# Kernel optimization log

Hardware: AMD Instinct MI355X
Metric: run time of the kernel (lower is better)

Reference implementation:

```python
import jax, jax.numpy as jnp
import numpy as np

B, D, E, H, O, TOP_K = 65536, 256, 16, 256, 256, 2
GATE_T = 1.0  # gate_temperature default


def setup_inputs() -> dict:
    key = jax.random.key(0)
    ks = jax.random.split(key, 8)
    sn = lambda k, shape, sc: (jax.random.normal(k, shape, jnp.float32) * sc)
    return {
        "x": sn(ks[0], (B, D), 1.0),
        # per-expert input bias, init N(0, 0.02) as in the module
        "bias": sn(ks[1], (E, D), 0.02),
        # expert MLP params: Linear(D,H) -> ReLU -> Linear(H,O), stacked over experts
        "W1": sn(ks[2], (E, D, H), 1.0 / np.sqrt(D)),
        "b1": jnp.zeros((E, H), jnp.float32),
        "W2": sn(ks[3], (E, H, O), 1.0 / np.sqrt(H)),
        "b2": jnp.zeros((E, O), jnp.float32),
        # gate MLP: Linear(D,4D) -> ReLU -> Linear(4D,D) -> ReLU -> Linear(D,E)
        "g1": sn(ks[4], (D, 4 * D), 1.0 / np.sqrt(D)),
        "gb1": jnp.zeros((4 * D,), jnp.float32),
        "g2": sn(ks[5], (4 * D, D), 1.0 / np.sqrt(4 * D)),
        "gb2": jnp.zeros((D,), jnp.float32),
        "g3": sn(ks[6], (D, E), 1.0 / np.sqrt(D)),
        "gb3": jnp.zeros((E,), jnp.float32),
    }


def reference(x, bias, W1, b1, W2, b2, g1, gb1, g2, gb2, g3, gb3):
    # --- gate ---
    h = jax.nn.relu(x @ g1 + gb1)
    h = jax.nn.relu(h @ g2 + gb2)
    gate_logits = h @ g3 + gb3              # [B, E]
    T = max(GATE_T, 1e-6)
    p = jax.nn.softmax(gate_logits / T, axis=1)

    # --- top-k sparsification + renormalize (top_k < num_experts) ---
    topv, topi = jax.lax.top_k(p, TOP_K)    # [B, K]
    rows = jnp.arange(p.shape[0])[:, None]
    p_sparse = jnp.zeros_like(p).at[rows, topi].set(topv)
    p = p_sparse / (p_sparse.sum(axis=1, keepdims=True) + 1e-9)

    # --- dense all-experts compute (module runs every expert on every token) ---
    xb = x[:, None, :] + bias[None]                                  # [B, E, D]
    he = jax.nn.relu(jnp.einsum("bed,edh->beh", xb, W1) + b1)      # [B, E, H]
    outs_all = jnp.einsum("beh,eho->beo", he, W2) + b2             # [B, E, O]

    # --- weighted combine (stopgrad_gate=False -> grads flow through p) ---
    y = jnp.einsum("be,beo->bo", p, outs_all)                      # [B, O]
    return (y, p)
```

## Files before the change

kernel.cpp:

```cpp
#include <hip/hip_runtime.h>
#include <cstdint>
#include <cstddef>

#define BTOK 65536
#define DDIM 256
#define NEXP 16
#define HDIM 256
#define ODIM 256
#define TAU2 1.2e-2f
#define TAU3 1.2e-4
#define AMB2_CAP 12288
#define AMB3_CAP 1024

typedef _Float16 fp16x8 __attribute__((ext_vector_type(8)));
typedef float    f32x4_t __attribute__((ext_vector_type(4)));

__device__ __forceinline__ void async_ld16(const void* g, void* l) {
  __builtin_amdgcn_global_load_lds(
      (const __attribute__((address_space(1))) unsigned int*)g,
      (__attribute__((address_space(3))) unsigned int*)l, 16, 0, 0);
}

__global__ __launch_bounds__(256) void k_transpose_cvt(
    const float* __restrict__ src, _Float16* __restrict__ dhi,
    _Float16* __restrict__ dlo, int R, int C) {
  __shared__ float s[32][33];
  int bz = blockIdx.z;
  size_t stride = (size_t)R * C;
  src += (size_t)bz * stride;
  dhi += (size_t)bz * stride;
  if (dlo) dlo += (size_t)bz * stride;
  int c0 = blockIdx.x * 32, r0 = blockIdx.y * 32;
  int tx = threadIdx.x & 31, ty = threadIdx.x >> 5;
  for (int k = 0; k < 32; k += 8)
    s[ty + k][tx] = src[(size_t)(r0 + ty + k) * C + c0 + tx];
  __syncthreads();
  for (int k = 0; k < 32; k += 8) {
    float v = s[tx][ty + k];
    _Float16 h = (_Float16)v;
    size_t o = (size_t)(c0 + ty + k) * R + r0 + tx;
    dhi[o] = h;
    if (dlo) dlo[o] = (_Float16)(v - (float)h);
  }
}

__global__ __launch_bounds__(256) void k_xcvt_hi(const float* __restrict__ x,
                                                 _Float16* __restrict__ xhi, int n8) {
  int i = blockIdx.x * 256 + threadIdx.x;
  if (i >= n8) return;
  const float4* p = (const float4*)x;
  float4 a = p[(size_t)i * 2], b = p[(size_t)i * 2 + 1];
  float v[8] = {a.x, a.y, a.z, a.w, b.x, b.y, b.z, b.w};
  fp16x8 hv;
#pragma unroll
  for (int j = 0; j < 8; j++) hv[j] = (_Float16)v[j];
  *(fp16x8*)(xhi + (size_t)i * 8) = hv;
}

__global__ __launch_bounds__(256) void k_gemm_f16(
    const _Float16* __restrict__ A, const _Float16* __restrict__ B,
    const float* __restrict__ bias, _Float16* __restrict__ C,
    int M, int N, int K) {
  __shared__ _Float16 sA[128 * 32], sB[128 * 32];
  const int tid = threadIdx.x;
  const int lane = tid & 63;
  const int wave = tid >> 6;
  const int wr = wave >> 1, wc = wave & 1;
  const int m0 = blockIdx.y * 128, n0 = blockIdx.x * 128;
  f32x4_t zero4 = {0.f, 0.f, 0.f, 0.f};
  f32x4_t acc[4][4];
#pragma unroll
  for (int i = 0; i < 4; i++)
#pragma unroll
    for (int j = 0; j < 4; j++) acc[i][j] = zero4;

  for (int k0 = 0; k0 < K; k0 += 32) {
#pragma unroll
    for (int r = 0; r < 2; r++) {
      int idx = r * 256 + tid;
      int row = idx >> 2, ch = idx & 3;
      int gch = ch ^ (row & 3);
      async_ld16(A + (size_t)(m0 + row) * K + k0 + gch * 8, &sA[idx * 8]);
      async_ld16(B + (size_t)(n0 + row) * K + k0 + gch * 8, &sB[idx * 8]);
    }
    __syncthreads();
    fp16x8 a[4], b[4];
    int kc = lane >> 4;
#pragma unroll
    for (int i = 0; i < 4; i++) {
      int ar = wr * 64 + i * 16 + (lane & 15);
      a[i] = *(const fp16x8*)&sA[ar * 32 + ((kc ^ (ar & 3)) << 3)];
      int br = wc * 64 + i * 16 + (lane & 15);
      b[i] = *(const fp16x8*)&sB[br * 32 + ((kc ^ (br & 3)) << 3)];
    }
#pragma unroll
    for (int i = 0; i < 4; i++)
#pragma unroll
      for (int j = 0; j < 4; j++)
        acc[i][j] = __builtin_amdgcn_mfma_f32_16x16x32_f16(a[i], b[j], acc[i][j], 0, 0, 0);
    __syncthreads();
  }
#pragma unroll
  for (int j = 0; j < 4; j++) {
    int col = n0 + wc * 64 + j * 16 + (lane & 15);
    float bc = bias[col];
#pragma unroll
    for (int i = 0; i < 4; i++)
#pragma unroll
      for (int q = 0; q < 4; q++) {
        int row = m0 + wr * 64 + i * 16 + ((lane >> 4) << 2) + q;
        float v = acc[i][j][q] + bc;
        v = v > 0.f ? v : 0.f;
        C[(size_t)row * N + col] = (_Float16)v;
      }
  }
}

__global__ __launch_bounds__(256) void k_gemm_split(
    const _Float16* __restrict__ Ahi, const _Float16* __restrict__ Alo,
    const _Float16* __restrict__ Bhi, const _Float16* __restrict__ Blo,
    const float* __restrict__ bias,
    _Float16* __restrict__ Chi, _Float16* __restrict__ Clo,
    int M, int N, int K, const int* __restrict__ nAct) {
  int nA = *nAct;
  if (nA > M) nA = M;
  const int m0 = blockIdx.y * 128, n0 = blockIdx.x * 128;
  if (m0 >= nA) return;
  __shared__ _Float16 sAh[128 * 32], sAl[128 * 32], sBh[128 * 32], sBl[128 * 32];
  const int tid = threadIdx.x;
  const int lane = tid & 63;
  const int wave = tid >> 6;
  const int wr = wave >> 1, wc = wave & 1;
  f32x4_t zero4 = {0.f, 0.f, 0.f, 0.f};
  f32x4_t acc[4][4];
#pragma unroll
  for (int i = 0; i < 4; i++)
#pragma unroll
    for (int j = 0; j < 4; j++) acc[i][j] = zero4;

  for (int k0 = 0; k0 < K; k0 += 32) {
#pragma unroll
    for (int r = 0; r < 2; r++) {
      int idx = r * 256 + tid;
      int row = idx >> 2, ch = idx & 3;
      int gch = ch ^ (row & 3);
      size_t ga = (size_t)(m0 + row) * K + k0 + gch * 8;
      size_t gb = (size_t)(n0 + row) * K + k0 + gch * 8;
      async_ld16(Ahi + ga, &sAh[idx * 8]);
      async_ld16(Alo + ga, &sAl[idx * 8]);
      async_ld16(Bhi + gb, &sBh[idx * 8]);
      async_ld16(Blo + gb, &sBl[idx * 8]);
    }
    __syncthreads();
    fp16x8 ah[4], al[4], bh[4], bl[4];
    int kc = lane >> 4;
#pragma unroll
    for (int i = 0; i < 4; i++) {
      int ar = wr * 64 + i * 16 + (lane & 15);
      int offa = ar * 32 + ((kc ^ (ar & 3)) << 3);
      ah[i] = *(const fp16x8*)&sAh[offa];
      al[i] = *(const fp16x8*)&sAl[offa];
      int br = wc * 64 + i * 16 + (lane & 15);
      int offb = br * 32 + ((kc ^ (br & 3)) << 3);
      bh[i] = *(const fp16x8*)&sBh[offb];
      bl[i] = *(const fp16x8*)&sBl[offb];
    }
#pragma unroll
    for (int i = 0; i < 4; i++)
#pragma unroll
      for (int j = 0; j < 4; j++) {
        acc[i][j] = __builtin_amdgcn_mfma_f32_16x16x32_f16(ah[i], bh[j], acc[i][j], 0, 0, 0);
        acc[i][j] = __builtin_amdgcn_mfma_f32_16x16x32_f16(ah[i], bl[j], acc[i][j], 0, 0, 0);
        acc[i][j] = __builtin_amdgcn_mfma_f32_16x16x32_f16(al[i], bh[j], acc[i][j], 0, 0, 0);
      }
    __syncthreads();
  }
#pragma unroll
  for (int j = 0; j < 4; j++) {
    int col = n0 + wc * 64 + j * 16 + (lane & 15);
    float bc = bias[col];
#pragma unroll
    for (int i = 0; i < 4; i++)
#pragma unroll
      for (int q = 0; q < 4; q++) {
        int row = m0 + wr * 64 + i * 16 + ((lane >> 4) << 2) + q;
        float v = acc[i][j][q] + bc;
        v = v > 0.f ? v : 0.f;
        _Float16 h = (_Float16)v;
        size_t o = (size_t)row * N + col;
        Chi[o] = h;
        Clo[o] = (_Float16)(v - (float)h);
      }
  }
}

__global__ __launch_bounds__(256) void k_gate3_fast(
    const _Float16* __restrict__ h2h, const float* __restrict__ g3,
    const float* __restrict__ gb3,
    float* __restrict__ pout, int* __restrict__ idx0, int* __restrict__ idx1,
    float* __restrict__ w0, float* __restrict__ w1,
    int* __restrict__ amb2Cnt, int* __restrict__ amb2List) {
  __shared__ _Float16 shh[16 * 256];
  __shared__ float sg3[16][260];
  __shared__ float sgb[16];
  __shared__ float slog[16][17];
  __shared__ int sidx[16][2];
  __shared__ float swv[16][2];
  int tid = threadIdx.x;
  int tokBase = blockIdx.x * 16;
  {
    int t = tid >> 4, c = (tid & 15) * 16;
    size_t g = (size_t)(tokBase + t) * 256 + c;
    *(fp16x8*)&shh[t * 256 + c] = *(const fp16x8*)&h2h[g];
    *(fp16x8*)&shh[t * 256 + c + 8] = *(const fp16x8*)&h2h[g + 8];
  }
#pragma unroll
  for (int r = 0; r < 16; r++) {
    int j = r * 256 + tid;
    sg3[j & 15][j >> 4] = g3[j];
  }
  if (tid < 16) sgb[tid] = gb3[tid];
  __syncthreads();
  int t = tid >> 4, e = tid & 15;
  const _Float16* ph = &shh[t * 256];
  const float* pg = &sg3[e][0];
  float acc = 0.f;
  for (int k = 0; k < 256; k += 8) {
    fp16x8 hv = *(const fp16x8*)&ph[k];
    float4 ga = *(const float4*)&pg[k];
    float4 gb = *(const float4*)&pg[k + 4];
    acc = fmaf((float)hv[0], ga.x, acc);
    acc = fmaf((float)hv[1], ga.y, acc);
    acc = fmaf((float)hv[2], ga.z, acc);
    acc = fmaf((float)hv[3], ga.w, acc);
    acc = fmaf((float)hv[4], gb.x, acc);
    acc = fmaf((float)hv[5], gb.y, acc);
    acc = fmaf((float)hv[6], gb.z, acc);
    acc = fmaf((float)hv[7], gb.w, acc);
  }
  acc += sgb[e];
  slog[t][e] = acc;
  __syncthreads();
  if (e == 0) {
    float l[16];
#pragma unroll
    for (int i = 0; i < 16; i++) l[i] = slog[t][i];
    int i1 = 0;
    for (int i = 1; i < 16; i++) if (l[i] > l[i1]) i1 = i;
    int i2 = -1;
    for (int i = 0; i < 16; i++) { if (i == i1) continue; if (i2 < 0 || l[i] > l[i2]) i2 = i; }
    float l3 = -1e30f;
    for (int i = 0; i < 16; i++) { if (i == i1 || i == i2) continue; if (l[i] > l3) l3 = l[i]; }
    float lmax = l[i1];
    float S = 0.f;
    for (int i = 0; i < 16; i++) S += expf(l[i] - lmax);
    float p1 = 1.0f / S, p2 = expf(l[i2] - lmax) / S;
    float den = p1 + p2 + 1e-9f;
    sidx[t][0] = i1; sidx[t][1] = i2;
    swv[t][0] = p1 / den; swv[t][1] = p2 / den;
    if (l[i2] - l3 < TAU2) {
      int pos = atomicAdd(amb2Cnt, 1);
      if (pos < AMB2_CAP) amb2List[pos] = tokBase + t;
    }
  }
  __syncthreads();
  int i1 = sidx[t][0], i2 = sidx[t][1];
  float pv = (e == i1) ? swv[t][0] : ((e == i2) ? swv[t][1] : 0.f);
  pout[(size_t)(tokBase + t) * 16 + e] = pv;
  if (e == 0) {
    int tok = tokBase + t;
    idx0[tok] = i1; idx1[tok] = i2;
    w0[tok] = swv[t][0]; w1[tok] = swv[t][1];
  }
}

__global__ __launch_bounds__(256) void k_gather2(
    const float* __restrict__ x, const int* __restrict__ cnt,
    const int* __restrict__ list,
    _Float16* __restrict__ xgh, _Float16* __restrict__ xgl) {
  int n = *cnt; if (n > AMB2_CAP) n = AMB2_CAP;
  int s = blockIdx.x * 8 + (threadIdx.x >> 5);
  if (s >= n) return;
  int tok = list[s];
  int c = (threadIdx.x & 31) * 8;
  const float4* p = (const float4*)&x[(size_t)tok * 256 + c];
  float4 a = p[0], b = p[1];
  float v[8] = {a.x, a.y, a.z, a.w, b.x, b.y, b.z, b.w};
  fp16x8 hv, lv;
#pragma unroll
  for (int j = 0; j < 8; j++) {
    _Float16 h = (_Float16)v[j];
    hv[j] = h;
    lv[j] = (_Float16)(v[j] - (float)h);
  }
  *(fp16x8*)&xgh[(size_t)s * 256 + c] = hv;
  *(fp16x8*)&xgl[(size_t)s * 256 + c] = lv;
}

__global__ __launch_bounds__(256) void k_gate3_precise(
    const _Float16* __restrict__ h2ghi, const _Float16* __restrict__ h2glo,
    const float* __restrict__ g3, const float* __restrict__ gb3,
    const int* __restrict__ amb2Cnt, const int* __restrict__ amb2List,
    float* __restrict__ pout, int* __restrict__ idx0, int* __restrict__ idx1,
    float* __restrict__ w0, float* __restrict__ w1,
    int* __restrict__ amb3Cnt, int* __restrict__ amb3List) {
  __shared__ _Float16 shh[16 * 256], shl[16 * 256];
  __shared__ float sg3[16][260];
  __shared__ float sgb[16];
  __shared__ double slog[16][17];
  __shared__ int sidx[16][2];
  __shared__ float swv[16][2];
  int tid = threadIdx.x;
  int slotBase = blockIdx.x * 16;
  int n2 = *amb2Cnt; if (n2 > AMB2_CAP) n2 = AMB2_CAP;
  {
    int t = tid >> 4, c = (tid & 15) * 16;
    size_t g = (size_t)(slotBase + t) * 256 + c;
    *(fp16x8*)&shh[t * 256 + c] = *(const fp16x8*)&h2ghi[g];
    *(fp16x8*)&shh[t * 256 + c + 8] = *(const fp16x8*)&h2ghi[g + 8];
    *(fp16x8*)&shl[t * 256 + c] = *(const fp16x8*)&h2glo[g];
    *(fp16x8*)&shl[t * 256 + c + 8] = *(const fp16x8*)&h2glo[g + 8];
  }
#pragma unroll
  for (int r = 0; r < 16; r++) {
    int j = r * 256 + tid;
    sg3[j & 15][j >> 4] = g3[j];
  }
  if (tid < 16) sgb[tid] = gb3[tid];
  __syncthreads();
  int t = tid >> 4, e = tid & 15;
  int slot = slotBase + t;
  const _Float16* ph = &shh[t * 256];
  const _Float16* pl = &shl[t * 256];
  const float* pg = &sg3[e][0];
  double acc = 0.0;
  for (int k = 0; k < 256; k += 4) {
#pragma unroll
    for (int j = 0; j < 4; j++) {
      double a = (double)(float)ph[k + j] + (double)(float)pl[k + j];
      acc = fma(a, (double)pg[k + j], acc);
    }
  }
  acc += (double)sgb[e];
  slog[t][e] = acc;
  __syncthreads();
  if (e == 0 && slot < n2) {
    double l[16];
#pragma unroll
    for (int i = 0; i < 16; i++) l[i] = slog[t][i];
    int i1 = 0;
    for (int i = 1; i < 16; i++) if (l[i] > l[i1]) i1 = i;
    int i2 = -1;
    for (int i = 0; i < 16; i++) { if (i == i1) continue; if (i2 < 0 || l[i] > l[i2]) i2 = i; }
    double l3 = -1e300;
    for (int i = 0; i < 16; i++) { if (i == i1 || i == i2) continue; if (l[i] > l3) l3 = l[i]; }
    double lmax = l[i1];
    double S = 0.0;
    for (int i = 0; i < 16; i++) S += exp(l[i] - lmax);
    double p1 = 1.0 / S, p2 = exp(l[i2] - lmax) / S;
    double den = p1 + p2 + 1e-9;
    sidx[t][0] = i1; sidx[t][1] = i2;
    swv[t][0] = (float)(p1 / den); swv[t][1] = (float)(p2 / den);
    if (l[i2] - l3 < TAU3) {
      int pos = atomicAdd(amb3Cnt, 1);
      if (pos < AMB3_CAP) amb3List[pos] = amb2List[slot];
    }
  }
  __syncthreads();
  if (slot < n2) {
    int tok = amb2List[slot];
    int i1 = sidx[t][0], i2 = sidx[t][1];
    float pv = (e == i1) ? swv[t][0] : ((e == i2) ? swv[t][1] : 0.f);
    pout[(size_t)tok * 16 + e] = pv;
    if (e == 0) {
      idx0[tok] = i1; idx1[tok] = i2;
      w0[tok] = swv[t][0]; w1[tok] = swv[t][1];
    }
  }
}

__global__ __launch_bounds__(256) void k_refine_par(
    const float* __restrict__ x,
    const float* __restrict__ g1, const float* __restrict__ gb1,
    const float* __restrict__ g2, const float* __restrict__ gb2,
    const float* __restrict__ g3, const float* __restrict__ gb3,
    const int* __restrict__ cnt, const int* __restrict__ list,
    float* __restrict__ pout, int* __restrict__ idx0, int* __restrict__ idx1,
    float* __restrict__ w0, float* __restrict__ w1) {
  __shared__ float sx[256];
  __shared__ double sh1[1024];
  __shared__ double sred[4][256];
  __shared__ double sh2[256];
  __shared__ double sl16[16][17];
  __shared__ int sidx[2];
  __shared__ float swv[2];
  int tid = threadIdx.x;
  int n = *cnt; if (n > AMB3_CAP) n = AMB3_CAP;
  for (int ii = blockIdx.x; ii < n; ii += gridDim.x) {
    int tok = list[ii];
    sx[tid] = x[(size_t)tok * 256 + tid];
    __syncthreads();
    {
      double a0 = 0, a1 = 0, a2 = 0, a3 = 0;
      const float* gp = g1 + tid * 4;
#pragma unroll 4
      for (int k = 0; k < 256; k++) {
        float4 gv = *(const float4*)(gp + (size_t)k * 1024);
        double xv = (double)sx[k];
        a0 = fma(xv, (double)gv.x, a0);
        a1 = fma(xv, (double)gv.y, a1);
        a2 = fma(xv, (double)gv.z, a2);
        a3 = fma(xv, (double)gv.w, a3);
      }
      double b0 = a0 + (double)gb1[tid * 4 + 0];
      double b1v = a1 + (double)gb1[tid * 4 + 1];
      double b2v = a2 + (double)gb1[tid * 4 + 2];
      double b3v = a3 + (double)gb1[tid * 4 + 3];
      sh1[tid * 4 + 0] = b0 > 0 ? b0 : 0.0;
      sh1[tid * 4 + 1] = b1v > 0 ? b1v : 0.0;
      sh1[tid * 4 + 2] = b2v > 0 ? b2v : 0.0;
      sh1[tid * 4 + 3] = b3v > 0 ? b3v : 0.0;
    }
    __syncthreads();
    {
      int p = tid >> 6, og = tid & 63;
      double a0 = 0, a1 = 0, a2 = 0, a3 = 0;
      const float* gp = g2 + og * 4 + (size_t)(p * 256) * 256;
      const double* hp = &sh1[p * 256];
#pragma unroll 4
      for (int k = 0; k < 256; k++) {
        float4 gv = *(const float4*)(gp + (size_t)k * 256);
        double hv = hp[k];
        a0 = fma(hv, (double)gv.x, a0);
        a1 = fma(hv, (double)gv.y, a1);
        a2 = fma(hv, (double)gv.z, a2);
        a3 = fma(hv, (double)gv.w, a3);
      }
      sred[p][og * 4 + 0] = a0;
      sred[p][og * 4 + 1] = a1;
      sred[p][og * 4 + 2] = a2;
      sred[p][og * 4 + 3] = a3;
    }
    __syncthreads();
    {
      double s = sred[0][tid] + sred[1][tid] + sred[2][tid] + sred[3][tid] + (double)gb2[tid];
      sh2[tid] = s > 0 ? s : 0.0;
    }
    __syncthreads();
    {
      int o = tid & 15, p = tid >> 4;
      double a = 0;
      const float* gp = g3 + o;
#pragma unroll
      for (int k = p * 16; k < p * 16 + 16; k++)
        a = fma(sh2[k], (double)gp[(size_t)k * 16], a);
      sl16[p][o] = a;
    }
    __syncthreads();
    if (tid == 0) {
      double l[16];
      for (int o = 0; o < 16; o++) {
        double a = (double)gb3[o];
        for (int p = 0; p < 16; p++) a += sl16[p][o];
        l[o] = a;
      }
      int i1 = 0;
      for (int i = 1; i < 16; i++) if (l[i] > l[i1]) i1 = i;
      int i2 = -1;
      for (int i = 0; i < 16; i++) { if (i == i1) continue; if (i2 < 0 || l[i] > l[i2]) i2 = i; }
      double lmax = l[i1];
      double S = 0.0;
      for (int i = 0; i < 16; i++) S += exp(l[i] - lmax);
      double p1 = 1.0 / S, p2 = exp(l[i2] - lmax) / S;
      double den = p1 + p2 + 1e-9;
      float fw0 = (float)(p1 / den), fw1 = (float)(p2 / den);
      sidx[0] = i1; sidx[1] = i2;
      swv[0] = fw0; swv[1] = fw1;
      idx0[tok] = i1; idx1[tok] = i2;
      w0[tok] = fw0; w1[tok] = fw1;
    }
    __syncthreads();
    if (tid < 16) {
      float pv = (tid == sidx[0]) ? swv[0] : ((tid == sidx[1]) ? swv[1] : 0.f);
      pout[(size_t)tok * 16 + tid] = pv;
    }
    __syncthreads();
  }
}

__global__ __launch_bounds__(256) void k_hist(const int* __restrict__ idx0,
                                              const int* __restrict__ idx1,
                                              int* __restrict__ cnt0, int* __restrict__ cnt1) {
  __shared__ int c0[16], c1[16];
  int tid = threadIdx.x;
  if (tid < 16) { c0[tid] = 0; c1[tid] = 0; }
  __syncthreads();
  int b = blockIdx.x * 256 + tid;
  atomicAdd(&c0[idx0[b]], 1);
  atomicAdd(&c1[idx1[b]], 1);
  __syncthreads();
  if (tid < 16) { atomicAdd(&cnt0[tid], c0[tid]); atomicAdd(&cnt1[tid], c1[tid]); }
}

__global__ void k_offsets(const int* __restrict__ cnt0, const int* __restrict__ cnt1,
                          int* off0, int* off1, int* cur0, int* cur1,
                          int* dExp0, int* dRow0, int* dExp1, int* dRow1, int* nTiles) {
  if (threadIdx.x == 0) {
    int tot = 0, nt = 0;
    for (int e = 0; e < 16; e++) {
      off0[e] = tot; cur0[e] = 0;
      int tiles = (cnt0[e] + 127) >> 7;
      for (int ti = 0; ti < tiles; ti++) { dExp0[nt] = e; dRow0[nt] = tot + ti * 128; nt++; }
      tot += tiles * 128;
    }
    nTiles[0] = nt;
    tot = 0; nt = 0;
    for (int e = 0; e < 16; e++) {
      off1[e] = tot; cur1[e] = 0;
      int tiles = (cnt1[e] + 127) >> 7;
      for (int ti = 0; ti < tiles; ti++) { dExp1[nt] = e; dRow1[nt] = tot + ti * 128; nt++; }
      tot += tiles * 128;
    }
    nTiles[1] = nt;
  }
}

__global__ __launch_bounds__(256) void k_scatter(
    const int* __restrict__ idx0, const int* __restrict__ idx1,
    const float* __restrict__ w0, const float* __restrict__ w1,
    const int* __restrict__ off0, const int* __restrict__ off1,
    int* cur0, int* cur1,
    int* __restrict__ tok0, float* __restrict__ wl0,
    int* __restrict__ tok1, float* __restrict__ wl1) {
  __shared__ int c0[16], c1[16], b0[16], b1[16];
  int tid = threadIdx.x;
  if (tid < 16) { c0[tid] = 0; c1[tid] = 0; }
  __syncthreads();
  int b = blockIdx.x * 256 + tid;
  int e0 = idx0[b], e1 = idx1[b];
  int r0 = atomicAdd(&c0[e0], 1);
  int r1 = atomicAdd(&c1[e1], 1);
  __syncthreads();
  if (tid < 16) { b0[tid] = atomicAdd(&cur0[tid], c0[tid]); b1[tid] = atomicAdd(&cur1[tid], c1[tid]); }
  __syncthreads();
  int p0 = off0[e0] + b0[e0] + r0;
  tok0[p0] = b; wl0[p0] = w0[b];
  int p1 = off1[e1] + b1[e1] + r1;
  tok1[p1] = b; wl1[p1] = w1[b];
}

template <int PASSB>
__global__ __launch_bounds__(512) void k_expert(
    const _Float16* __restrict__ xhi, const float* __restrict__ bias,
    const _Float16* __restrict__ W1T, const float* __restrict__ b1,
    const _Float16* __restrict__ W2T, const float* __restrict__ b2,
    const int* __restrict__ dExp, const int* __restrict__ dRow,
    const int* __restrict__ nT,
    const int* __restrict__ tokL, const float* __restrict__ wL,
    float* __restrict__ y) {
  __shared__ _Float16 sA[128 * 64];
  __shared__ _Float16 sB[256 * 64];
  __shared__ _Float16 sHE[128 * 264];
  __shared__ int sTok[128];
  __shared__ float sW[128];
  int tid = threadIdx.x, lane = tid & 63, wave = tid >> 6;
  int wr = wave >> 2, wc = wave & 3;
  f32x4_t zero4 = {0.f, 0.f, 0.f, 0.f};
  int nt = *nT;
  for (int t = blockIdx.x; t < nt; t += gridDim.x) {
    int e = dExp[t], rowOff = dRow[t];
    if (tid < 128) { sTok[tid] = tokL[rowOff + tid]; sW[tid] = wL[rowOff + tid]; }
    __syncthreads();
    f32x4_t acc[4][4];
#pragma unroll
    for (int i = 0; i < 4; i++)
#pragma unroll
      for (int j = 0; j < 4; j++) acc[i][j] = zero4;
    const _Float16* W1e = W1T + (size_t)e * 65536;
    const _Float16* W2e = W2T + (size_t)e * 65536;
    const float* be = bias + e * 256;
    for (int k0 = 0; k0 < 256; k0 += 64) {
#pragma unroll
      for (int r = 0; r < 2; r++) {
        int idx = r * 512 + tid;
        int row = idx >> 3, ch = idx & 7, gch = ch ^ (row & 7);
        int tok = sTok[row];
        int tk = tok < 0 ? 0 : tok;
        fp16x8 v = *(const fp16x8*)&xhi[(size_t)tk * 256 + k0 + gch * 8];
        const float* bp = &be[k0 + gch * 8];
#pragma unroll
        for (int j = 0; j < 8; j++) v[j] = (_Float16)((float)v[j] + bp[j]);
        *(fp16x8*)&sA[row * 64 + ch * 8] = v;
      }
#pragma unroll
      for (int r = 0; r < 4; r++) {
        int idx = r * 512 + tid;
        int row = idx >> 3, ch = idx & 7, gch = ch ^ (row & 7);
        *(fp16x8*)&sB[row * 64 + ch * 8] =
            *(const fp16x8*)&W1e[(size_t)row * 256 + k0 + gch * 8];
      }
      __syncthreads();
#pragma unroll
      for (int kk = 0; kk < 2; kk++) {
        fp16x8 a[4], bf[4];
        int kcg = kk * 4 + (lane >> 4);
#pragma unroll
        for (int i = 0; i < 4; i++) {
          int ar = wr * 64 + i * 16 + (lane & 15);
          a[i] = *(const fp16x8*)&sA[ar * 64 + (kcg ^ (ar & 7)) * 8];
          int br = wc * 64 + i * 16 + (lane & 15);
          bf[i] = *(const fp16x8*)&sB[br * 64 + (kcg ^ (br & 7)) * 8];
        }
#pragma unroll
        for (int i = 0; i < 4; i++)
#pragma unroll
          for (int j = 0; j < 4; j++)
            acc[i][j] = __builtin_amdgcn_mfma_f32_16x16x32_f16(a[i], bf[j], acc[i][j], 0, 0, 0);
      }
      __syncthreads();
    }
#pragma unroll
    for (int j = 0; j < 4; j++) {
      int col = wc * 64 + j * 16 + (lane & 15);
      float bb = b1[e * 256 + col];
#pragma unroll
      for (int i = 0; i < 4; i++)
#pragma unroll
        for (int q = 0; q < 4; q++) {
          int row = wr * 64 + i * 16 + ((lane >> 4) << 2) + q;
          float v = acc[i][j][q] + bb;
          v = v > 0.f ? v : 0.f;
          sHE[row * 264 + col] = (_Float16)v;
        }
    }
#pragma unroll
    for (int i = 0; i < 4; i++)
#pragma unroll
      for (int j = 0; j < 4; j++) acc[i][j] = zero4;
    __syncthreads();
    for (int k0 = 0; k0 < 256; k0 += 64) {
#pragma unroll
      for (int r = 0; r < 4; r++) {
        int idx = r * 512 + tid;
        int row = idx >> 3, ch = idx & 7, gch = ch ^ (row & 7);
        *(fp16x8*)&sB[row * 64 + ch * 8] =
            *(const fp16x8*)&W2e[(size_t)row * 256 + k0 + gch * 8];
      }
      __syncthreads();
#pragma unroll
      for (int kk = 0; kk < 2; kk++) {
        fp16x8 a[4], bf[4];
        int kcg = kk * 4 + (lane >> 4);
#pragma unroll
        for (int i = 0; i < 4; i++) {
          int ar = wr * 64 + i * 16 + (lane & 15);
          a[i] = *(const fp16x8*)&sHE[ar * 264 + k0 + kk * 32 + (lane >> 4) * 8];
          int br = wc * 64 + i * 16 + (lane & 15);
          bf[i] = *(const fp16x8*)&sB[br * 64 + (kcg ^ (br & 7)) * 8];
        }
#pragma unroll
        for (int i = 0; i < 4; i++)
#pragma unroll
          for (int j = 0; j < 4; j++)
            acc[i][j] = __builtin_amdgcn_mfma_f32_16x16x32_f16(a[i], bf[j], acc[i][j], 0, 0, 0);
      }
      __syncthreads();
    }
#pragma unroll
    for (int j = 0; j < 4; j++) {
      int col = wc * 64 + j * 16 + (lane & 15);
      float bb = b2[e * 256 + col];
#pragma unroll
      for (int i = 0; i < 4; i++)
#pragma unroll
        for (int q = 0; q < 4; q++) {
          int row = wr * 64 + i * 16 + ((lane >> 4) << 2) + q;
          int tok = sTok[row];
          if (tok >= 0) {
            float v = (acc[i][j][q] + bb) * sW[row];
            size_t o = (size_t)tok * 256 + col;
            if (PASSB) y[o] += v; else y[o] = v;
          }
        }
    }
    __syncthreads();
  }
}

extern "C" void kernel_launch(void* const* d_in, const int* in_sizes, int n_in,
                              void* d_out, int out_size, void* d_ws, size_t ws_size,
                              hipStream_t stream) {
  const float* x   = (const float*)d_in[0];
  const float* bias= (const float*)d_in[1];
  const float* W1  = (const float*)d_in[2];
  const float* b1  = (const float*)d_in[3];
  const float* W2  = (const float*)d_in[4];
  const float* b2  = (const float*)d_in[5];
  const float* g1  = (const float*)d_in[6];
  const float* gb1 = (const float*)d_in[7];
  const float* g2  = (const float*)d_in[8];
  const float* gb2 = (const float*)d_in[9];
  const float* g3  = (const float*)d_in[10];
  const float* gb3 = (const float*)d_in[11];
  float* y    = (float*)d_out;
  float* pout = y + (size_t)BTOK * 256;

  char* w = (char*)d_ws;
  auto alloc = [&](size_t bytes) -> char* {
    char* p = w;
    w += (bytes + 255) & ~(size_t)255;
    return p;
  };
  _Float16* xhi  = (_Float16*)alloc((size_t)BTOK * 256 * 2);
  _Float16* h2h  = (_Float16*)alloc((size_t)BTOK * 256 * 2);
  _Float16* g1Th = (_Float16*)alloc((size_t)256 * 1024 * 2);
  _Float16* g1Tl = (_Float16*)alloc((size_t)256 * 1024 * 2);
  _Float16* g2Th = (_Float16*)alloc((size_t)256 * 1024 * 2);
  _Float16* g2Tl = (_Float16*)alloc((size_t)256 * 1024 * 2);
  _Float16* W1T  = (_Float16*)alloc((size_t)16 * 65536 * 2);
  _Float16* W2T  = (_Float16*)alloc((size_t)16 * 65536 * 2);
  int*   idx0 = (int*)alloc((size_t)BTOK * 4);
  int*   idx1 = (int*)alloc((size_t)BTOK * 4);
  float* w0a  = (float*)alloc((size_t)BTOK * 4);
  float* w1a  = (float*)alloc((size_t)BTOK * 4);
  int*   ctrl = (int*)alloc(4096);
  int*   amb2List = (int*)alloc((size_t)AMB2_CAP * 4);
  int*   amb3List = (int*)alloc((size_t)AMB3_CAP * 4);
  int*   dExp0 = (int*)alloc(544 * 4);
  int*   dRow0 = (int*)alloc(544 * 4);
  int*   dExp1 = (int*)alloc(544 * 4);
  int*   dRow1 = (int*)alloc(544 * 4);
  const int LCAP = BTOK + 16 * 128;
  int*   tok0 = (int*)alloc((size_t)LCAP * 4);
  float* wl0  = (float*)alloc((size_t)LCAP * 4);
  int*   tok1 = (int*)alloc((size_t)LCAP * 4);
  float* wl1  = (float*)alloc((size_t)LCAP * 4);
  _Float16* xgh  = (_Float16*)alloc((size_t)AMB2_CAP * 256 * 2);
  _Float16* xgl  = (_Float16*)alloc((size_t)AMB2_CAP * 256 * 2);
  _Float16* h1gh = (_Float16*)alloc((size_t)AMB2_CAP * 1024 * 2);
  _Float16* h1gl = (_Float16*)alloc((size_t)AMB2_CAP * 1024 * 2);
  _Float16* h2gh = (_Float16*)alloc((size_t)AMB2_CAP * 256 * 2);
  _Float16* h2gl = (_Float16*)alloc((size_t)AMB2_CAP * 256 * 2);

  size_t used = (size_t)(w - (char*)d_ws);
  size_t remain = ws_size > used ? ws_size - used : 0;
  int CG = 1;
  while (CG < 64 && (size_t)(BTOK / CG) * 1024 * 2 + 1024 > remain) CG <<= 1;
  int MC = BTOK / CG;
  _Float16* h1h = (_Float16*)alloc((size_t)MC * 1024 * 2);

  int* cnt0 = ctrl + 0;  int* cnt1 = ctrl + 16;
  int* off0 = ctrl + 32; int* off1 = ctrl + 48;
  int* cur0 = ctrl + 64; int* cur1 = ctrl + 80;
  int* nTiles = ctrl + 96;
  int* amb2Cnt = ctrl + 112;
  int* amb3Cnt = ctrl + 116;

  hipMemsetAsync(ctrl, 0, 4096, stream);
  hipMemsetAsync(tok0, 0xFF, (size_t)LCAP * 4, stream);
  hipMemsetAsync(tok1, 0xFF, (size_t)LCAP * 4, stream);

  dim3 tb(256);
  k_transpose_cvt<<<dim3(32, 8, 1), tb, 0, stream>>>(g1, g1Th, g1Tl, 256, 1024);
  k_transpose_cvt<<<dim3(8, 32, 1), tb, 0, stream>>>(g2, g2Th, g2Tl, 1024, 256);
  k_transpose_cvt<<<dim3(8, 8, 16), tb, 0, stream>>>(W1, W1T, nullptr, 256, 256);
  k_transpose_cvt<<<dim3(8, 8, 16), tb, 0, stream>>>(W2, W2T, nullptr, 256, 256);
  k_xcvt_hi<<<(BTOK * 256 / 8 + 255) / 256, tb, 0, stream>>>(x, xhi, BTOK * 256 / 8);

  for (int c = 0; c < CG; c++) {
    const _Float16* xh = xhi + (size_t)c * MC * 256;
    k_gemm_f16<<<dim3(8, MC / 128), tb, 0, stream>>>(xh, g1Th, gb1, h1h, MC, 1024, 256);
    k_gemm_f16<<<dim3(2, MC / 128), tb, 0, stream>>>(h1h, g2Th, gb2,
                                                     h2h + (size_t)c * MC * 256, MC, 256, 1024);
  }
  k_gate3_fast<<<BTOK / 16, tb, 0, stream>>>(h2h, g3, gb3, pout, idx0, idx1,
                                             w0a, w1a, amb2Cnt, amb2List);

  k_gather2<<<AMB2_CAP / 8, tb, 0, stream>>>(x, amb2Cnt, amb2List, xgh, xgl);
  k_gemm_split<<<dim3(8, AMB2_CAP / 128), tb, 0, stream>>>(
      xgh, xgl, g1Th, g1Tl, gb1, h1gh, h1gl, AMB2_CAP, 1024, 256, amb2Cnt);
  k_gemm_split<<<dim3(2, AMB2_CAP / 128), tb, 0, stream>>>(
      h1gh, h1gl, g2Th, g2Tl, gb2, h2gh, h2gl, AMB2_CAP, 256, 1024, amb2Cnt);
  k_gate3_precise<<<AMB2_CAP / 16, tb, 0, stream>>>(
      h2gh, h2gl, g3, gb3, amb2Cnt, amb2List, pout, idx0, idx1, w0a, w1a,
      amb3Cnt, amb3List);

  k_refine_par<<<512, tb, 0, stream>>>(x, g1, gb1, g2, gb2, g3, gb3,
                                       amb3Cnt, amb3List, pout, idx0, idx1, w0a, w1a);

  k_hist<<<BTOK / 256, tb, 0, stream>>>(idx0, idx1, cnt0, cnt1);
  k_offsets<<<1, 64, 0, stream>>>(cnt0, cnt1, off0, off1, cur0, cur1,
                                  dExp0, dRow0, dExp1, dRow1, nTiles);
  k_scatter<<<BTOK / 256, tb, 0, stream>>>(idx0, idx1, w0a, w1a, off0, off1,
                                           cur0, cur1, tok0, wl0, tok1, wl1);
  k_expert<0><<<528, 512, 0, stream>>>(xhi, bias, W1T, b1, W2T, b2,
                                       dExp0, dRow0, nTiles + 0, tok0, wl0, y);
  k_expert<1><<<528, 512, 0, stream>>>(xhi, bias, W1T, b1, W2T, b2,
                                       dExp1, dRow1, nTiles + 1, tok1, wl1, y);
}
```

Measured before the change: 807.5 us.

## Split fp64 refine into three parallel layer kernels and fuse histogram into gating

The single refine kernel, which looped over ambiguous tokens with one block each, is replaced by three kernels (layer1, layer2, layer3). Each spreads a token's fp64 matmul across many blocks and writes intermediates to new global buffers. The separate expert histogram kernel is removed: counts are accumulated in the fast gate kernel and corrected with atomic decrement/increment when the precise or refine stages change a token's expert choice. This trades an extra full pass over the indices and a serial per-token refine loop for more kernel launches, fp64 intermediate traffic, and more atomics.

```diff
diff --git a/kernel.cpp b/kernel.cpp
--- a/kernel.cpp
+++ b/kernel.cpp
@@ -199,15 +199,18 @@
     const float* __restrict__ gb3,
     float* __restrict__ pout, int* __restrict__ idx0, int* __restrict__ idx1,
     float* __restrict__ w0, float* __restrict__ w1,
-    int* __restrict__ amb2Cnt, int* __restrict__ amb2List) {
+    int* __restrict__ amb2Cnt, int* __restrict__ amb2List,
+    int* __restrict__ cnt0, int* __restrict__ cnt1) {
   __shared__ _Float16 shh[16 * 256];
   __shared__ float sg3[16][260];
   __shared__ float sgb[16];
   __shared__ float slog[16][17];
   __shared__ int sidx[16][2];
   __shared__ float swv[16][2];
+  __shared__ int hc0[16], hc1[16];
   int tid = threadIdx.x;
   int tokBase = blockIdx.x * 16;
+  if (tid < 16) { hc0[tid] = 0; hc1[tid] = 0; }
   {
     int t = tid >> 4, c = (tid & 15) * 16;
     size_t g = (size_t)(tokBase + t) * 256 + c;
@@ -258,6 +261,8 @@
     float den = p1 + p2 + 1e-9f;
     sidx[t][0] = i1; sidx[t][1] = i2;
     swv[t][0] = p1 / den; swv[t][1] = p2 / den;
+    atomicAdd(&hc0[i1], 1);
+    atomicAdd(&hc1[i2], 1);
     if (l[i2] - l3 < TAU2) {
       int pos = atomicAdd(amb2Cnt, 1);
       if (pos < AMB2_CAP) amb2List[pos] = tokBase + t;
@@ -271,6 +276,10 @@
     int tok = tokBase + t;
     idx0[tok] = i1; idx1[tok] = i2;
     w0[tok] = swv[t][0]; w1[tok] = swv[t][1];
+  }
+  if (tid < 16) {
+    if (hc0[tid]) atomicAdd(&cnt0[tid], hc0[tid]);
+    if (hc1[tid]) atomicAdd(&cnt1[tid], hc1[tid]);
   }
 }
 
@@ -303,7 +312,8 @@
     const int* __restrict__ amb2Cnt, const int* __restrict__ amb2List,
     float* __restrict__ pout, int* __restrict__ idx0, int* __restrict__ idx1,
     float* __restrict__ w0, float* __restrict__ w1,
-    int* __restrict__ amb3Cnt, int* __restrict__ amb3List) {
+    int* __restrict__ amb3Cnt, int* __restrict__ amb3List,
+    int* __restrict__ cnt0, int* __restrict__ cnt1) {
   __shared__ _Float16 shh[16 * 256], shl[16 * 256];
   __shared__ float sg3[16][260];
   __shared__ float sgb[16];
@@ -345,6 +355,7 @@
   slog[t][e] = acc;
   __syncthreads();
   if (e == 0 && slot < n2) {
+    int tok = amb2List[slot];
     double l[16];
 #pragma unroll
     for (int i = 0; i < 16; i++) l[i] = slog[t][i];
@@ -361,9 +372,12 @@
     double den = p1 + p2 + 1e-9;
     sidx[t][0] = i1; sidx[t][1] = i2;
     swv[t][0] = (float)(p1 / den); swv[t][1] = (float)(p2 / den);
+    int o0 = idx0[tok], o1 = idx1[tok];
+    if (i1 != o0) { atomicSub(&cnt0[o0], 1); atomicAdd(&cnt0[i1], 1); }
+    if (i2 != o1) { atomicSub(&cnt1[o1], 1); atomicAdd(&cnt1[i2], 1); }
     if (l[i2] - l3 < TAU3) {
       int pos = atomicAdd(amb3Cnt, 1);
-      if (pos < AMB3_CAP) amb3List[pos] = amb2List[slot];
+      if (pos < AMB3_CAP) amb3List[pos] = tok;
     }
   }
   __syncthreads();
@@ -379,127 +393,123 @@
   }
 }
 
-__global__ __launch_bounds__(256) void k_refine_par(
-    const float* __restrict__ x,
-    const float* __restrict__ g1, const float* __restrict__ gb1,
-    const float* __restrict__ g2, const float* __restrict__ gb2,
-    const float* __restrict__ g3, const float* __restrict__ gb3,
+__global__ __launch_bounds__(256) void k_ref_l1(
+    const float* __restrict__ x, const float* __restrict__ g1,
+    const float* __restrict__ gb1,
+    const int* __restrict__ cnt, const int* __restrict__ list,
+    double* __restrict__ h1d) {
+  int n = *cnt; if (n > AMB3_CAP) n = AMB3_CAP;
+  int t = blockIdx.y;
+  if (t >= n) return;
+  __shared__ float sx[256];
+  __shared__ double sred[4][64];
+  int tid = threadIdx.x;
+  int tok = list[t];
+  sx[tid] = x[(size_t)tok * 256 + tid];
+  __syncthreads();
+  int o = tid & 63, p = tid >> 6;
+  int out = blockIdx.x * 64 + o;
+  double a = 0.0;
+  const float* gp = g1 + (size_t)(p * 64) * 1024 + out;
+  const float* xp = &sx[p * 64];
+#pragma unroll 8
+  for (int k = 0; k < 64; k++)
+    a = fma((double)xp[k], (double)gp[(size_t)k * 1024], a);
+  sred[p][o] = a;
+  __syncthreads();
+  if (p == 0) {
+    double s = sred[0][o] + sred[1][o] + sred[2][o] + sred[3][o] + (double)gb1[out];
+    h1d[(size_t)t * 1024 + out] = s > 0.0 ? s : 0.0;
+  }
+}
+
+__global__ __launch_bounds__(512) void k_ref_l2(
+    const double* __restrict__ h1d, const float* __restrict__ g2,
+    const float* __restrict__ gb2,
+    const int* __restrict__ cnt, double* __restrict__ h2d) {
+  int n = *cnt; if (n > AMB3_CAP) n = AMB3_CAP;
+  int t = blockIdx.y;
+  if (t >= n) return;
+  __shared__ double sh1[1024];
+  __shared__ double sred[8][64];
+  int tid = threadIdx.x;
+  sh1[tid] = h1d[(size_t)t * 1024 + tid];
+  sh1[512 + tid] = h1d[(size_t)t * 1024 + 512 + tid];
+  __syncthreads();
+  int o = tid & 63, p = tid >> 6;
+  int out = blockIdx.x * 64 + o;
+  double a = 0.0;
+  const float* gp = g2 + (size_t)(p * 128) * 256 + out;
+  const double* hp = &sh1[p * 128];
+#pragma unroll 4
+  for (int k = 0; k < 128; k++)
+    a = fma(hp[k], (double)gp[(size_t)k * 256], a);
+  sred[p][o] = a;
+  __syncthreads();
+  if (p == 0) {
+    double s = sred[0][o] + sred[1][o] + sred[2][o] + sred[3][o] +
+               sred[4][o] + sred[5][o] + sred[6][o] + sred[7][o] + (double)gb2[out];
+    h2d[(size_t)t * 256 + out] = s > 0.0 ? s : 0.0;
+  }
+}
+
+__global__ __launch_bounds__(256) void k_ref_l3(
+    const double* __restrict__ h2d, const float* __restrict__ g3,
+    const float* __restrict__ gb3,
     const int* __restrict__ cnt, const int* __restrict__ list,
     float* __restrict__ pout, int* __restrict__ idx0, int* __restrict__ idx1,
-    float* __restrict__ w0, float* __restrict__ w1) {
-  __shared__ float sx[256];
-  __shared__ double sh1[1024];
-  __shared__ double sred[4][256];
+    float* __restrict__ w0, float* __restrict__ w1,
+    int* __restrict__ cnt0, int* __restrict__ cnt1) {
+  int n = *cnt; if (n > AMB3_CAP) n = AMB3_CAP;
+  int t = blockIdx.x;
+  if (t >= n) return;
   __shared__ double sh2[256];
   __shared__ double sl16[16][17];
   __shared__ int sidx[2];
   __shared__ float swv[2];
   int tid = threadIdx.x;
-  int n = *cnt; if (n > AMB3_CAP) n = AMB3_CAP;
-  for (int ii = blockIdx.x; ii < n; ii += gridDim.x) {
-    int tok = list[ii];
-    sx[tid] = x[(size_t)tok * 256 + tid];
-    __syncthreads();
-    {
-      double a0 = 0, a1 = 0, a2 = 0, a3 = 0;
-      const float* gp = g1 + tid * 4;
-#pragma unroll 4
-      for (int k = 0; k < 256; k++) {
-        float4 gv = *(const float4*)(gp + (size_t)k * 1024);
-        double xv = (double)sx[k];
-        a0 = fma(xv, (double)gv.x, a0);
-        a1 = fma(xv, (double)gv.y, a1);
-        a2 = fma(xv, (double)gv.z, a2);
-        a3 = fma(xv, (double)gv.w, a3);
-      }
-      double b0 = a0 + (double)gb1[tid * 4 + 0];
-      double b1v = a1 + (double)gb1[tid * 4 + 1];
-      double b2v = a2 + (double)gb1[tid * 4 + 2];
-      double b3v = a3 + (double)gb1[tid * 4 + 3];
-      sh1[tid * 4 + 0] = b0 > 0 ? b0 : 0.0;
-      sh1[tid * 4 + 1] = b1v > 0 ? b1v : 0.0;
-      sh1[tid * 4 + 2] = b2v > 0 ? b2v : 0.0;
-      sh1[tid * 4 + 3] = b3v > 0 ? b3v : 0.0;
-    }
-    __syncthreads();
-    {
-      int p = tid >> 6, og = tid & 63;
-      double a0 = 0, a1 = 0, a2 = 0, a3 = 0;
-      const float* gp = g2 + og * 4 + (size_t)(p * 256) * 256;
-      const double* hp = &sh1[p * 256];
-#pragma unroll 4
-      for (int k = 0; k < 256; k++) {
-        float4 gv = *(const float4*)(gp + (size_t)k * 256);
-        double hv = hp[k];
-        a0 = fma(hv, (double)gv.x, a0);
-        a1 = fma(hv, (double)gv.y, a1);
-        a2 = fma(hv, (double)gv.z, a2);
-        a3 = fma(hv, (double)gv.w, a3);
-      }
-      sred[p][og * 4 + 0] = a0;
-      sred[p][og * 4 + 1] = a1;
-      sred[p][og * 4 + 2] = a2;
-      sred[p][og * 4 + 3] = a3;
-    }
-    __syncthreads();
-    {
-      double s = sred[0][tid] + sred[1][tid] + sred[2][tid] + sred[3][tid] + (double)gb2[tid];
-      sh2[tid] = s > 0 ? s : 0.0;
-    }
-    __syncthreads();
-    {
-      int o = tid & 15, p = tid >> 4;
-      double a = 0;
-      const float* gp = g3 + o;
-#pragma unroll
-      for (int k = p * 16; k < p * 16 + 16; k++)
-        a = fma(sh2[k], (double)gp[(size_t)k * 16], a);
-      sl16[p][o] = a;
-    }
-    __syncthreads();
-    if (tid == 0) {
-      double l[16];
-      for (int o = 0; o < 16; o++) {
-        double a = (double)gb3[o];
-        for (int p = 0; p < 16; p++) a += sl16[p][o];
-        l[o] = a;
-      }
-      int i1 = 0;
-      for (int i = 1; i < 16; i++) if (l[i] > l[i1]) i1 = i;
-      int i2 = -1;
-      for (int i = 0; i < 16; i++) { if (i == i1) continue; if (i2 < 0 || l[i] > l[i2]) i2 = i; }
-      double lmax = l[i1];
-      double S = 0.0;
-      for (int i = 0; i < 16; i++) S += exp(l[i] - lmax);
-      double p1 = 1.0 / S, p2 = exp(l[i2] - lmax) / S;
-      double den = p1 + p2 + 1e-9;
-      float fw0 = (float)(p1 / den), fw1 = (float)(p2 / den);
-      sidx[0] = i1; sidx[1] = i2;
-      swv[0] = fw0; swv[1] = fw1;
-      idx0[tok] = i1; idx1[tok] = i2;
-      w0[tok] = fw0; w1[tok] = fw1;
-    }
-    __syncthreads();
-    if (tid < 16) {
-      float pv = (tid == sidx[0]) ? swv[0] : ((tid == sidx[1]) ? swv[1] : 0.f);
-      pout[(size_t)tok * 16 + tid] = pv;
-    }
-    __syncthreads();
-  }
-}
-
-__global__ __launch_bounds__(256) void k_hist(const int* __restrict__ idx0,
-                                              const int* __restrict__ idx1,
-                                              int* __restrict__ cnt0, int* __restrict__ cnt1) {
-  __shared__ int c0[16], c1[16];
-  int tid = threadIdx.x;
-  if (tid < 16) { c0[tid] = 0; c1[tid] = 0; }
-  __syncthreads();
-  int b = blockIdx.x * 256 + tid;
-  atomicAdd(&c0[idx0[b]], 1);
-  atomicAdd(&c1[idx1[b]], 1);
-  __syncthreads();
-  if (tid < 16) { atomicAdd(&cnt0[tid], c0[tid]); atomicAdd(&cnt1[tid], c1[tid]); }
+  int tok = list[t];
+  sh2[tid] = h2d[(size_t)t * 256 + tid];
+  __syncthreads();
+  {
+    int o = tid & 15, pp = tid >> 4;
+    double a = 0.0;
+#pragma unroll
+    for (int k = pp * 16; k < pp * 16 + 16; k++)
+      a = fma(sh2[k], (double)g3[(size_t)k * 16 + o], a);
+    sl16[pp][o] = a;
+  }
+  __syncthreads();
+  if (tid == 0) {
+    double l[16];
+    for (int o = 0; o < 16; o++) {
+      double a = (double)gb3[o];
+      for (int p = 0; p < 16; p++) a += sl16[p][o];
+      l[o] = a;
+    }
+    int i1 = 0;
+    for (int i = 1; i < 16; i++) if (l[i] > l[i1]) i1 = i;
+    int i2 = -1;
+    for (int i = 0; i < 16; i++) { if (i == i1) continue; if (i2 < 0 || l[i] > l[i2]) i2 = i; }
+    double lmax = l[i1];
+    double S = 0.0;
+    for (int i = 0; i < 16; i++) S += exp(l[i] - lmax);
+    double p1 = 1.0 / S, p2 = exp(l[i2] - lmax) / S;
+    double den = p1 + p2 + 1e-9;
+    float fw0 = (float)(p1 / den), fw1 = (float)(p2 / den);
+    int o0 = idx0[tok], o1 = idx1[tok];
+    if (i1 != o0) { atomicSub(&cnt0[o0], 1); atomicAdd(&cnt0[i1], 1); }
+    if (i2 != o1) { atomicSub(&cnt1[o1], 1); atomicAdd(&cnt1[i2], 1); }
+    sidx[0] = i1; sidx[1] = i2;
+    swv[0] = fw0; swv[1] = fw1;
+    idx0[tok] = i1; idx1[tok] = i2;
+    w0[tok] = fw0; w1[tok] = fw1;
+  }
+  __syncthreads();
+  if (tid < 16) {
+    float pv = (tid == sidx[0]) ? swv[0] : ((tid == sidx[1]) ? swv[1] : 0.f);
+    pout[(size_t)tok * 16 + tid] = pv;
+  }
 }
 
 __global__ void k_offsets(const int* __restrict__ cnt0, const int* __restrict__ cnt1,
@@ -741,6 +751,8 @@
   _Float16* h1gl = (_Float16*)alloc((size_t)AMB2_CAP * 1024 * 2);
   _Float16* h2gh = (_Float16*)alloc((size_t)AMB2_CAP * 256 * 2);
   _Float16* h2gl = (_Float16*)alloc((size_t)AMB2_CAP * 256 * 2);
+  double* h1d = (double*)alloc((size_t)AMB3_CAP * 1024 * 8);
+  double* h2d = (double*)alloc((size_t)AMB3_CAP * 256 * 8);
 
   size_t used = (size_t)(w - (char*)d_ws);
   size_t remain = ws_size > used ? ws_size - used : 0;
@@ -774,7 +786,7 @@
                                                      h2h + (size_t)c * MC * 256, MC, 256, 1024);
   }
   k_gate3_fast<<<BTOK / 16, tb, 0, stream>>>(h2h, g3, gb3, pout, idx0, idx1,
-                                             w0a, w1a, amb2Cnt, amb2List);
+                                             w0a, w1a, amb2Cnt, amb2List, cnt0, cnt1);
 
   k_gather2<<<AMB2_CAP / 8, tb, 0, stream>>>(x, amb2Cnt, amb2List, xgh, xgl);
   k_gemm_split<<<dim3(8, AMB2_CAP / 128), tb, 0, stream>>>(
@@ -783,12 +795,13 @@
       h1gh, h1gl, g2Th, g2Tl, gb2, h2gh, h2gl, AMB2_CAP, 256, 1024, amb2Cnt);
   k_gate3_precise<<<AMB2_CAP / 16, tb, 0, stream>>>(
       h2gh, h2gl, g3, gb3, amb2Cnt, amb2List, pout, idx0, idx1, w0a, w1a,
-      amb3Cnt, amb3List);
-
-  k_refine_par<<<512, tb, 0, stream>>>(x, g1, gb1, g2, gb2, g3, gb3,
-                                       amb3Cnt, amb3List, pout, idx0, idx1, w0a, w1a);
-
-  k_hist<<<BTOK / 256, tb, 0, stream>>>(idx0, idx1, cnt0, cnt1);
+      amb3Cnt, amb3List, cnt0, cnt1);
+
+  k_ref_l1<<<dim3(16, AMB3_CAP), tb, 0, stream>>>(x, g1, gb1, amb3Cnt, amb3List, h1d);
+  k_ref_l2<<<dim3(4, AMB3_CAP), 512, 0, stream>>>(h1d, g2, gb2, amb3Cnt, h2d);
+  k_ref_l3<<<AMB3_CAP, tb, 0, stream>>>(h2d, g3, gb3, amb3Cnt, amb3List,
+                                        pout, idx0, idx1, w0a, w1a, cnt0, cnt1);
+
   k_offsets<<<1, 64, 0, stream>>>(cnt0, cnt1, off0, off1, cur0, cur1,
                                   dExp0, dRow0, dExp1, dRow1, nTiles);
   k_scatter<<<BTOK / 256, tb, 0, stream>>>(idx0, idx1, w0a, w1a, off0, off1,
```

New measurement: 686.0 us. -15.0%, faster.
